# Performance work log

Hardware: AMD Instinct MI355X
Metric: run time of the kernel (lower is better)

Reference implementation:

```python
import jax, jax.numpy as jnp
import numpy as np

TAU_PLUS = 0.1
BETA = 1.0
TEMPERATURE = 0.5
EPS = 1e-8


def setup_inputs() -> dict:
    key = jax.random.key(0)
    B = 4096
    logits = jax.random.normal(key, (B, B), dtype=jnp.float32)
    return {"logits": logits}


def reference(logits):
    B = logits.shape[0]
    t = TEMPERATURE
    N = 2 * B - 2

    # positive pairs: diagonal twice
    d = jnp.diagonal(logits)
    pos = jnp.exp(jnp.concatenate([d, d]) / t)  # [2B]

    # 2B x 2B block similarity matrix [[L, L^T], [L^T, L]]
    sim = jnp.block([[logits, logits.T], [logits.T, logits]])

    # analytic negative mask: exclude diagonal and the paired entry (|i-j| == B)
    idx = jnp.arange(2 * B)
    diff = jnp.abs(idx[:, None] - idx[None, :])
    mask = (diff != 0) & (diff != B)  # [2B, 2B] bool, N true per row

    neg = jnp.where(mask, jnp.exp(sim / t), 0.0)  # masked entries contribute 0

    # hard-negative reweighting: imp = exp(beta * log(neg)) = neg**beta on kept entries
    safe_neg = jnp.where(mask, neg, 1.0)  # avoid log(0)
    imp = jnp.where(mask, jnp.exp(BETA * jnp.log(safe_neg)), 0.0)
    # torch mean over N kept columns == sum / N
    reweight_neg = (imp * neg).sum(axis=1) / (imp.sum(axis=1) / N)

    Ng = (-TAU_PLUS * N * pos + reweight_neg) / (1.0 - TAU_PLUS)
    Ng = jnp.maximum(Ng, N * jnp.exp(jnp.asarray(-1.0 / t, dtype=logits.dtype)))

    loss = -jnp.log(pos / (pos + Ng + EPS))
    return loss.mean()
```

## Files before the change

### kernel.cpp

```cpp
#include <hip/hip_runtime.h>
#include <math.h>


#define THREADS    256
#define EXP_SCALE  2.885390081777927f

__global__ __launch_bounds__(THREADS) void pass1_kernel(
    const float* __restrict__ L,
    float* __restrict__ rowPE,
    float* __restrict__ rowPE2,
    float* __restrict__ colPE,
    float* __restrict__ colPE2,
    int B)
{
    const int lane    = threadIdx.x & 63;
    const int wave    = threadIdx.x >> 6;
    const int x       = blockIdx.x;
    const int stripe  = blockIdx.y * 4 + wave;
    const int row0    = stripe * 4;
    const int colBase = x * 1024 + lane * 4;

    float cE[16], cE2[16];
#pragma unroll
    for (int k = 0; k < 16; ++k) { cE[k] = 0.f; cE2[k] = 0.f; }

#pragma unroll
    for (int r = 0; r < 4; ++r) {
        const float* Lr = L + (size_t)(row0 + r) * B + colBase;
        float rs = 0.f, rs2 = 0.f;
#pragma unroll
        for (int j = 0; j < 4; ++j) {
            const float4 v = *reinterpret_cast<const float4*>(Lr + j * 256);
            float e0 = exp2f(v.x * EXP_SCALE);
            float e1 = exp2f(v.y * EXP_SCALE);
            float e2 = exp2f(v.z * EXP_SCALE);
            float e3 = exp2f(v.w * EXP_SCALE);
            float q0 = e0 * e0, q1 = e1 * e1, q2 = e2 * e2, q3 = e3 * e3;
            cE [j * 4 + 0] += e0; cE [j * 4 + 1] += e1;
            cE [j * 4 + 2] += e2; cE [j * 4 + 3] += e3;
            cE2[j * 4 + 0] += q0; cE2[j * 4 + 1] += q1;
            cE2[j * 4 + 2] += q2; cE2[j * 4 + 3] += q3;
            rs  += (e0 + e1) + (e2 + e3);
            rs2 += (q0 + q1) + (q2 + q3);
        }
#pragma unroll
        for (int off = 32; off > 0; off >>= 1) {
            rs  += __shfl_down(rs,  off, 64);
            rs2 += __shfl_down(rs2, off, 64);
        }
        if (lane == 0) {
            rowPE [(size_t)x * B + row0 + r] = rs;
            rowPE2[(size_t)x * B + row0 + r] = rs2;
        }
    }

    float* cpe  = colPE  + (size_t)stripe * B + colBase;
    float* cpe2 = colPE2 + (size_t)stripe * B + colBase;
#pragma unroll
    for (int j = 0; j < 4; ++j) {
        *reinterpret_cast<float4*>(cpe  + j * 256) =
            make_float4(cE [j*4+0], cE [j*4+1], cE [j*4+2], cE [j*4+3]);
        *reinterpret_cast<float4*>(cpe2 + j * 256) =
            make_float4(cE2[j*4+0], cE2[j*4+1], cE2[j*4+2], cE2[j*4+3]);
    }
}

__global__ __launch_bounds__(THREADS) void pass2_kernel(
    const float* __restrict__ L,
    const float* __restrict__ rowPE,
    const float* __restrict__ rowPE2,
    const float* __restrict__ colPE,
    const float* __restrict__ colPE2,
    float* __restrict__ out,
    int B, int S)
{
    const int t    = threadIdx.x;
    const int lane = t & 63;
    const int wave = t >> 6;
    const int col  = blockIdx.x * 64 + lane;

    float se = 0.f, se2 = 0.f;
    const int k0 = wave * (S / 4), k1 = k0 + (S / 4);
#pragma unroll 8
    for (int k = k0; k < k1; ++k) {
        se  += colPE [(size_t)k * B + col];
        se2 += colPE2[(size_t)k * B + col];
    }
    __shared__ float2 part[4][64];
    part[wave][lane] = make_float2(se, se2);
    __syncthreads();

    if (wave == 0) {
        float colE  = (part[0][lane].x + part[1][lane].x) + (part[2][lane].x + part[3][lane].x);
        float colE2 = (part[0][lane].y + part[1][lane].y) + (part[2][lane].y + part[3][lane].y);
        const int i = col;
        float rowE  = (rowPE [i] + rowPE [B + i]) + (rowPE [2*B + i] + rowPE [3*B + i]);
        float rowE2 = (rowPE2[i] + rowPE2[B + i]) + (rowPE2[2*B + i] + rowPE2[3*B + i]);

        const float Nf = (float)(2 * B - 2);
        float dg = L[(size_t)i * B + i];
        float pe = exp2f(dg * EXP_SCALE);
        float S1 = rowE  + colE  - 2.f * pe;
        float S2 = rowE2 + colE2 - 2.f * (pe * pe);
        float rw = Nf * (S2 / S1);
        float Ng = (rw - 0.1f * Nf * pe) * (1.f / 0.9f);
        Ng = fmaxf(Ng, Nf * 0.13533528323661270f);
        float loss = logf((pe + Ng + 1e-8f) / pe);
#pragma unroll
        for (int off = 32; off > 0; off >>= 1) loss += __shfl_down(loss, off, 64);
        if (lane == 0) atomicAdd(out, loss / (float)B);
    }
}

extern "C" void kernel_launch(void* const* d_in, const int* in_sizes, int n_in,
                              void* d_out, int out_size, void* d_ws, size_t ws_size,
                              hipStream_t stream) {
    const float* L = (const float*)d_in[0];
    int B = 1;
    while ((long long)B * B < (long long)in_sizes[0]) B <<= 1;
    const int S = B / 4;

    float* rowPE  = (float*)d_ws;
    float* rowPE2 = rowPE  + (size_t)4 * B;
    float* colPE  = rowPE2 + (size_t)4 * B;
    float* colPE2 = colPE  + (size_t)S * B;

    hipMemsetAsync(d_out, 0, sizeof(float), stream);

    dim3 grid1(4, B / 16);
    pass1_kernel<<<grid1, THREADS, 0, stream>>>(L, rowPE, rowPE2, colPE, colPE2, B);
    pass2_kernel<<<B / 64, THREADS, 0, stream>>>(L, rowPE, rowPE2, colPE, colPE2,
                                                 (float*)d_out, B, S);
}
```

Before: 111.3 us.

## Reduce column partials in LDS per block and interleave sums as float2

```diff
diff --git a/kernel.cpp b/kernel.cpp
--- a/kernel.cpp
+++ b/kernel.cpp
@@ -7,27 +7,29 @@
 
 __global__ __launch_bounds__(THREADS) void pass1_kernel(
     const float* __restrict__ L,
-    float* __restrict__ rowPE,
-    float* __restrict__ rowPE2,
-    float* __restrict__ colPE,
-    float* __restrict__ colPE2,
+    float2* __restrict__ rowP,
+    float2* __restrict__ colP,
     int B)
 {
-    const int lane    = threadIdx.x & 63;
-    const int wave    = threadIdx.x >> 6;
+    __shared__ float ldsE [4][1024];
+    __shared__ float ldsE2[4][1024];
+
+    const int t       = threadIdx.x;
+    const int lane    = t & 63;
+    const int wave    = t >> 6;
     const int x       = blockIdx.x;
-    const int stripe  = blockIdx.y * 4 + wave;
-    const int row0    = stripe * 4;
+    const int s       = blockIdx.y;
+    const int row0    = s * 16 + wave * 4;
     const int colBase = x * 1024 + lane * 4;
 
-    float cE[16], cE2[16];
+    float cE[16], cE2[16], rs[4], rs2[4];
 #pragma unroll
     for (int k = 0; k < 16; ++k) { cE[k] = 0.f; cE2[k] = 0.f; }
 
 #pragma unroll
     for (int r = 0; r < 4; ++r) {
         const float* Lr = L + (size_t)(row0 + r) * B + colBase;
-        float rs = 0.f, rs2 = 0.f;
+        float a = 0.f, b = 0.f;
 #pragma unroll
         for (int j = 0; j < 4; ++j) {
             const float4 v = *reinterpret_cast<const float4*>(Lr + j * 256);
@@ -36,67 +38,78 @@
             float e2 = exp2f(v.z * EXP_SCALE);
             float e3 = exp2f(v.w * EXP_SCALE);
             float q0 = e0 * e0, q1 = e1 * e1, q2 = e2 * e2, q3 = e3 * e3;
-            cE [j * 4 + 0] += e0; cE [j * 4 + 1] += e1;
-            cE [j * 4 + 2] += e2; cE [j * 4 + 3] += e3;
-            cE2[j * 4 + 0] += q0; cE2[j * 4 + 1] += q1;
-            cE2[j * 4 + 2] += q2; cE2[j * 4 + 3] += q3;
-            rs  += (e0 + e1) + (e2 + e3);
-            rs2 += (q0 + q1) + (q2 + q3);
+            cE [j*4+0] += e0; cE [j*4+1] += e1; cE [j*4+2] += e2; cE [j*4+3] += e3;
+            cE2[j*4+0] += q0; cE2[j*4+1] += q1; cE2[j*4+2] += q2; cE2[j*4+3] += q3;
+            a += (e0 + e1) + (e2 + e3);
+            b += (q0 + q1) + (q2 + q3);
         }
+        rs[r] = a; rs2[r] = b;
+    }
+
+#pragma unroll
+    for (int r = 0; r < 4; ++r) {
+        float a = rs[r], b = rs2[r];
 #pragma unroll
         for (int off = 32; off > 0; off >>= 1) {
-            rs  += __shfl_down(rs,  off, 64);
-            rs2 += __shfl_down(rs2, off, 64);
+            a += __shfl_down(a, off, 64);
+            b += __shfl_down(b, off, 64);
         }
-        if (lane == 0) {
-            rowPE [(size_t)x * B + row0 + r] = rs;
-            rowPE2[(size_t)x * B + row0 + r] = rs2;
-        }
+        if (lane == 0) rowP[(size_t)x * B + row0 + r] = make_float2(a, b);
     }
 
-    float* cpe  = colPE  + (size_t)stripe * B + colBase;
-    float* cpe2 = colPE2 + (size_t)stripe * B + colBase;
 #pragma unroll
     for (int j = 0; j < 4; ++j) {
-        *reinterpret_cast<float4*>(cpe  + j * 256) =
+        *reinterpret_cast<float4*>(&ldsE [wave][lane * 4 + j * 256]) =
             make_float4(cE [j*4+0], cE [j*4+1], cE [j*4+2], cE [j*4+3]);
-        *reinterpret_cast<float4*>(cpe2 + j * 256) =
+        *reinterpret_cast<float4*>(&ldsE2[wave][lane * 4 + j * 256]) =
             make_float4(cE2[j*4+0], cE2[j*4+1], cE2[j*4+2], cE2[j*4+3]);
+    }
+    __syncthreads();
+
+#pragma unroll
+    for (int m = 0; m < 4; ++m) {
+        const int c = t + m * 256;
+        float se  = (ldsE [0][c] + ldsE [1][c]) + (ldsE [2][c] + ldsE [3][c]);
+        float se2 = (ldsE2[0][c] + ldsE2[1][c]) + (ldsE2[2][c] + ldsE2[3][c]);
+        colP[(size_t)s * B + x * 1024 + c] = make_float2(se, se2);
     }
 }
 
 __global__ __launch_bounds__(THREADS) void pass2_kernel(
     const float* __restrict__ L,
-    const float* __restrict__ rowPE,
-    const float* __restrict__ rowPE2,
-    const float* __restrict__ colPE,
-    const float* __restrict__ colPE2,
+    const float2* __restrict__ rowP,
+    const float2* __restrict__ colP,
     float* __restrict__ out,
     int B, int S)
 {
     const int t    = threadIdx.x;
-    const int lane = t & 63;
-    const int wave = t >> 6;
-    const int col  = blockIdx.x * 64 + lane;
+    const int c    = t & 15;
+    const int g    = t >> 4;
+    const int base = blockIdx.x * 16;
 
     float se = 0.f, se2 = 0.f;
-    const int k0 = wave * (S / 4), k1 = k0 + (S / 4);
-#pragma unroll 8
-    for (int k = k0; k < k1; ++k) {
-        se  += colPE [(size_t)k * B + col];
-        se2 += colPE2[(size_t)k * B + col];
+    for (int k = g; k < S; k += 16) {
+        const float2 v = colP[(size_t)k * B + base + c];
+        se += v.x; se2 += v.y;
     }
-    __shared__ float2 part[4][64];
-    part[wave][lane] = make_float2(se, se2);
+    __shared__ float2 part[16][17];
+    part[g][c] = make_float2(se, se2);
     __syncthreads();
 
-    if (wave == 0) {
-        float colE  = (part[0][lane].x + part[1][lane].x) + (part[2][lane].x + part[3][lane].x);
-        float colE2 = (part[0][lane].y + part[1][lane].y) + (part[2][lane].y + part[3][lane].y);
-        const int i = col;
-        float rowE  = (rowPE [i] + rowPE [B + i]) + (rowPE [2*B + i] + rowPE [3*B + i]);
-        float rowE2 = (rowPE2[i] + rowPE2[B + i]) + (rowPE2[2*B + i] + rowPE2[3*B + i]);
-
+    if (t < 16) {
+        float colE = 0.f, colE2 = 0.f;
+#pragma unroll
+        for (int gg = 0; gg < 16; ++gg) {
+            colE  += part[gg][t].x;
+            colE2 += part[gg][t].y;
+        }
+        const int i = base + t;
+        float rowE = 0.f, rowE2 = 0.f;
+#pragma unroll
+        for (int x = 0; x < 4; ++x) {
+            const float2 rv = rowP[(size_t)x * B + i];
+            rowE += rv.x; rowE2 += rv.y;
+        }
         const float Nf = (float)(2 * B - 2);
         float dg = L[(size_t)i * B + i];
         float pe = exp2f(dg * EXP_SCALE);
@@ -107,8 +120,8 @@
         Ng = fmaxf(Ng, Nf * 0.13533528323661270f);
         float loss = logf((pe + Ng + 1e-8f) / pe);
 #pragma unroll
-        for (int off = 32; off > 0; off >>= 1) loss += __shfl_down(loss, off, 64);
-        if (lane == 0) atomicAdd(out, loss / (float)B);
+        for (int off = 8; off > 0; off >>= 1) loss += __shfl_down(loss, off, 16);
+        if (t == 0) atomicAdd(out, loss / (float)B);
     }
 }
 
@@ -118,17 +131,14 @@
     const float* L = (const float*)d_in[0];
     int B = 1;
     while ((long long)B * B < (long long)in_sizes[0]) B <<= 1;
-    const int S = B / 4;
+    const int S = B / 16;
 
-    float* rowPE  = (float*)d_ws;
-    float* rowPE2 = rowPE  + (size_t)4 * B;
-    float* colPE  = rowPE2 + (size_t)4 * B;
-    float* colPE2 = colPE  + (size_t)S * B;
+    float2* rowP = (float2*)d_ws;
+    float2* colP = rowP + (size_t)4 * B;
 
     hipMemsetAsync(d_out, 0, sizeof(float), stream);
 
     dim3 grid1(4, B / 16);
-    pass1_kernel<<<grid1, THREADS, 0, stream>>>(L, rowPE, rowPE2, colPE, colPE2, B);
-    pass2_kernel<<<B / 64, THREADS, 0, stream>>>(L, rowPE, rowPE2, colPE, colPE2,
-                                                 (float*)d_out, B, S);
+    pass1_kernel<<<grid1, THREADS, 0, stream>>>(L, rowP, colP, B);
+    pass2_kernel<<<B / 16, THREADS, 0, stream>>>(L, rowP, colP, (float*)d_out, B, S);
 }
```

Result: faster. 100.9 us (-9.3%).
